# Kernel tuning notes

Measured on AMD Instinct MI355X. Metric: run time of the kernel, lower is better.

## Reference

```python
import jax, jax.numpy as jnp
import numpy as np

N_NODES = 50000
N_EDGES = 400000
N_GRAPHS = 128
D_IN = 768
D_HID = 256
D_OUT = 256
EPS_COS = 1e-8
EPS_BN = 1e-5
NEG_SLOPE = 0.2  # PyG GATConv default


def setup_inputs() -> dict:
    key = jax.random.key(0)
    ks = jax.random.split(key, 16)
    inp = {
        "claim_emb": jax.random.normal(ks[0], (N_GRAPHS, D_IN), dtype=jnp.float32),
        "x": jax.random.normal(ks[1], (N_NODES, D_IN), dtype=jnp.float32),
        "edge_index": jax.random.randint(ks[2], (2, N_EDGES), 0, N_NODES, dtype=jnp.int64 if jax.config.jax_enable_x64 else jnp.int32),
        "node_batch": jnp.sort(jax.random.randint(ks[3], (N_NODES,), 0, N_GRAPHS, dtype=jnp.int64 if jax.config.jax_enable_x64 else jnp.int32)),
        # GAT layer 1 (768 -> 256, single head)
        "W1": jax.random.normal(ks[4], (D_IN, D_HID), dtype=jnp.float32) * (1.0 / np.sqrt(D_IN)),
        "a_src1": jax.random.normal(ks[5], (D_HID,), dtype=jnp.float32) * 0.1,
        "a_dst1": jax.random.normal(ks[6], (D_HID,), dtype=jnp.float32) * 0.1,
        "b1": jnp.zeros((D_HID,), dtype=jnp.float32),
        # GAT layer 2 (256 -> 256)
        "W2": jax.random.normal(ks[7], (D_HID, D_OUT), dtype=jnp.float32) * (1.0 / np.sqrt(D_HID)),
        "a_src2": jax.random.normal(ks[8], (D_OUT,), dtype=jnp.float32) * 0.1,
        "a_dst2": jax.random.normal(ks[9], (D_OUT,), dtype=jnp.float32) * 0.1,
        "b2": jnp.zeros((D_OUT,), dtype=jnp.float32),
        # BatchNorm after layer 1
        "bn_gamma": jnp.ones((D_HID,), dtype=jnp.float32),
        "bn_beta": jnp.zeros((D_HID,), dtype=jnp.float32),
        # classifier: (gnn_out + claim_dim) -> 1
        "clf_W": jax.random.normal(ks[10], (D_OUT + D_IN, 1), dtype=jnp.float32) * (1.0 / np.sqrt(D_OUT + D_IN)),
        "clf_b": jnp.zeros((1,), dtype=jnp.float32),
    }
    return inp


def _gat_conv(x, src, dst, n_nodes, W, a_src, a_dst, b):
    """PyG GATConv, heads=1, concat=True, self-loops already appended to src/dst."""
    h = x @ W                                  # [N, H]
    alpha_s = h @ a_src                        # [N]
    alpha_d = h @ a_dst                        # [N]
    e = jax.nn.leaky_relu(alpha_s[src] + alpha_d[dst], NEG_SLOPE)  # [E]
    # segment softmax over edges grouped by destination node
    m = jax.ops.segment_max(e, dst, num_segments=n_nodes)          # [N]
    ex = jnp.exp(e - m[dst])
    denom = jax.ops.segment_sum(ex, dst, num_segments=n_nodes)     # [N]
    attn = ex / denom[dst]                                         # [E]
    out = jax.ops.segment_sum(h[src] * attn[:, None], dst, num_segments=n_nodes)
    return out + b


def reference(claim_emb, x, edge_index, node_batch,
              W1, a_src1, a_dst1, b1, W2, a_src2, a_dst2, b2,
              bn_gamma, bn_beta, clf_W, clf_b):
    n_nodes = x.shape[0]
    n_graphs = claim_emb.shape[0]

    # relevance weighting: cosine similarity between claim (per node's graph) and node feature
    ce = claim_emb[node_batch]                                      # [N, 768]
    dot = jnp.sum(ce * x, axis=-1)
    norm = jnp.linalg.norm(ce, axis=-1) * jnp.linalg.norm(x, axis=-1)
    rel = dot / jnp.maximum(norm, EPS_COS)                          # [N]
    h = x * rel[:, None]

    # add self loops (PyG GATConv default)
    loops = jnp.arange(n_nodes, dtype=edge_index.dtype)
    src = jnp.concatenate([edge_index[0], loops])
    dst = jnp.concatenate([edge_index[1], loops])

    # layer 1: GAT -> BatchNorm (training-mode batch stats) -> ReLU
    h = _gat_conv(h, src, dst, n_nodes, W1, a_src1, a_dst1, b1)
    mu = jnp.mean(h, axis=0)
    var = jnp.var(h, axis=0)
    h = (h - mu) / jnp.sqrt(var + EPS_BN) * bn_gamma + bn_beta
    h = jax.nn.relu(h)

    # layer 2: GAT -> ReLU
    h = _gat_conv(h, src, dst, n_nodes, W2, a_src2, a_dst2, b2)
    h = jax.nn.relu(h)

    # global mean pool per graph
    sums = jax.ops.segment_sum(h, node_batch, num_segments=n_graphs)            # [B, 256]
    counts = jax.ops.segment_sum(jnp.ones((n_nodes,), h.dtype), node_batch, num_segments=n_graphs)
    pooled = sums / jnp.maximum(counts, 1.0)[:, None]

    combined = jnp.concatenate([pooled, claim_emb], axis=1)                     # [B, 256+768]
    out = combined @ clf_W + clf_b                                              # [B, 1]
    return out[:, 0]
```

## Files before the change

### kernel.cpp

```cpp
#include <hip/hip_runtime.h>
#include <hip/hip_bf16.h>

#define N_NODES  50000
#define N_EDGES  400000
#define E_TOT    450000
#define N_GRAPHS 128
#define D_IN     768
#define D_HID    256

typedef __hip_bfloat16 bf16;
typedef __attribute__((ext_vector_type(8))) short short8;
typedef __attribute__((ext_vector_type(4))) short short4v;
typedef __attribute__((ext_vector_type(4))) float f32x4;

__device__ __forceinline__ float b2f(bf16 v) { return __bfloat162float(v); }
__device__ __forceinline__ float us2f(unsigned short u) { return __uint_as_float((unsigned)u << 16); }
__device__ __forceinline__ int clampN(int v) { return min(max(v, 0), N_NODES - 1); }
__device__ __forceinline__ short f2bs(float f) {
  unsigned u = __float_as_uint(f);
  return (short)((u + 0x7FFFu + ((u >> 16) & 1u)) >> 16);
}

__device__ __forceinline__ void gload_lds16(const void* g, void* l) {
  __builtin_amdgcn_global_load_lds(
      (const __attribute__((address_space(1))) void*)g,
      (__attribute__((address_space(3))) void*)l, 16, 0, 0);
}

__device__ __forceinline__ float waveReduceSum(float v) {
#pragma unroll
  for (int o = 32; o > 0; o >>= 1) v += __shfl_down(v, o);
  return v;
}

__device__ __forceinline__ float blockReduce256(float v, volatile float* buf4) {
  int lane = threadIdx.x & 63, wid = threadIdx.x >> 6;
  v = waveReduceSum(v);
  if (lane == 0) buf4[wid] = v;
  __syncthreads();
  float s = buf4[0] + buf4[1] + buf4[2] + buf4[3];
  __syncthreads();
  return s;
}

__global__ __launch_bounds__(256) void detect_idx_kernel(
    const int* __restrict__ edge32, int* __restrict__ flagNZ) {
  int t = threadIdx.x;
  int nz = 0;
#pragma unroll
  for (int i = 0; i < 4; ++i) {
    int idx = 2 * (t + i * 256) + 1;
    if (edge32[idx] != 0) nz = 1;
  }
  if (nz) atomicOr(flagNZ, 1);
}

__global__ __launch_bounds__(256) void normalize_idx_kernel(
    const void* __restrict__ edge, const void* __restrict__ nbin,
    const int* __restrict__ flagNZ,
    int* __restrict__ src32, int* __restrict__ dst32, int* __restrict__ nb32) {
  bool is64 = (*flagNZ == 0);
  long i = (long)blockIdx.x * 256 + threadIdx.x;
  const int*       e32 = (const int*)edge;
  const long long* e64 = (const long long*)edge;
  const int*       n32 = (const int*)nbin;
  const long long* n64 = (const long long*)nbin;
  if (i < N_EDGES) {
    src32[i] = clampN(is64 ? (int)e64[i] : e32[i]);
    dst32[i] = clampN(is64 ? (int)e64[N_EDGES + i] : e32[N_EDGES + i]);
  }
  long j = i - N_EDGES;
  if (j >= 0 && j < N_NODES)
    nb32[j] = min(max(is64 ? (int)n64[j] : n32[j], 0), N_GRAPHS - 1);
}

__global__ __launch_bounds__(256) void hist_kernel(
    const int* __restrict__ dst, int* __restrict__ deg) {
  int i = blockIdx.x * 256 + threadIdx.x;
  if (i >= E_TOT) return;
  int d = (i < N_EDGES) ? dst[i] : (i - N_EDGES);
  atomicAdd(&deg[d], 1);
}

#define SCAN_VPT 4
#define SCAN_BLK (256 * SCAN_VPT)
#define SCAN_NB  ((N_NODES + SCAN_BLK - 1) / SCAN_BLK)

__global__ __launch_bounds__(256) void scan_local_kernel(
    const int* __restrict__ deg, int* __restrict__ incl, int* __restrict__ blockSums) {
  __shared__ int wsum[4];
  int lane = threadIdx.x & 63, wid = threadIdx.x >> 6;
  int tbase = blockIdx.x * SCAN_BLK + threadIdx.x * SCAN_VPT;
  int v[SCAN_VPT];
  int s = 0;
#pragma unroll
  for (int j = 0; j < SCAN_VPT; ++j) {
    int i = tbase + j;
    v[j] = (i < N_NODES) ? deg[i] : 0;
    s += v[j];
  }
  int sc = s;
#pragma unroll
  for (int o = 1; o < 64; o <<= 1) {
    int t = __shfl_up(sc, o);
    if (lane >= o) sc += t;
  }
  if (lane == 63) wsum[wid] = sc;
  __syncthreads();
  int woff = 0;
  for (int w = 0; w < wid; ++w) woff += wsum[w];
  int run = woff + sc - s;
#pragma unroll
  for (int j = 0; j < SCAN_VPT; ++j) {
    run += v[j];
    int i = tbase + j;
    if (i < N_NODES) incl[i] = run;
  }
  if (threadIdx.x == 255)
    blockSums[blockIdx.x] = woff + sc;
}

__global__ __launch_bounds__(256) void scan_spine_kernel(int* __restrict__ bs) {
  __shared__ int wsum[4];
  int lane = threadIdx.x & 63, wid = threadIdx.x >> 6;
  int v = (threadIdx.x < SCAN_NB) ? bs[threadIdx.x] : 0;
  int sc = v;
#pragma unroll
  for (int o = 1; o < 64; o <<= 1) {
    int t = __shfl_up(sc, o);
    if (lane >= o) sc += t;
  }
  if (lane == 63) wsum[wid] = sc;
  __syncthreads();
  int woff = 0;
  for (int w = 0; w < wid; ++w) woff += wsum[w];
  if (threadIdx.x < SCAN_NB) bs[threadIdx.x] = woff + sc - v;
}

__global__ __launch_bounds__(256) void scan_add_kernel(
    const int* __restrict__ deg, const int* __restrict__ incl,
    const int* __restrict__ blockOffs,
    int* __restrict__ rowptr, int* __restrict__ pos) {
  int i = blockIdx.x * 256 + threadIdx.x;
  if (i >= N_NODES) return;
  int ic = incl[i] + blockOffs[i / SCAN_BLK];
  rowptr[i + 1] = ic;
  pos[i] = ic - deg[i];
  if (i == 0) rowptr[0] = 0;
}

__global__ __launch_bounds__(256) void scatter_kernel(
    const int* __restrict__ src, const int* __restrict__ dst,
    int* __restrict__ pos, int* __restrict__ srcS) {
  int i = blockIdx.x * 256 + threadIdx.x;
  if (i >= E_TOT) return;
  int s, d;
  if (i < N_EDGES) { s = src[i]; d = dst[i]; } else { s = d = i - N_EDGES; }
  int j = atomicAdd(&pos[d], 1);
  srcS[j] = s;
}

__global__ __launch_bounds__(256) void convert_wt_kernel(
    const float* __restrict__ W, short* __restrict__ WT, int K, int N) {
  int i = blockIdx.x * 256 + threadIdx.x;
  if (i >= K * N) return;
  int n = i / K, k = i - n * K;
  WT[i] = f2bs(W[(size_t)k * N + n]);
}

__global__ __launch_bounds__(256) void rel_conv_kernel(
    const float* __restrict__ x, const float* __restrict__ claim,
    const int* __restrict__ nb, short* __restrict__ Abf) {
  __shared__ float buf[4];
  int n = blockIdx.x;
  int g = nb[n];
  const float* xr = x + (size_t)n * D_IN;
  const float* cr = claim + (size_t)g * D_IN;
  float xv[3];
  float dot = 0.f, nx = 0.f, nc = 0.f;
#pragma unroll
  for (int i = 0; i < 3; ++i) {
    int d = threadIdx.x + i * 256;
    xv[i] = xr[d];
    float cv = cr[d];
    dot += xv[i] * cv; nx += xv[i] * xv[i]; nc += cv * cv;
  }
  dot = blockReduce256(dot, buf);
  nx  = blockReduce256(nx, buf);
  nc  = blockReduce256(nc, buf);
  float rel = dot / fmaxf(sqrtf(nx) * sqrtf(nc), 1e-8f);
#pragma unroll
  for (int i = 0; i < 3; ++i)
    Abf[(size_t)n * D_IN + threadIdx.x + i * 256] = f2bs(xv[i] * rel);
}

__global__ __launch_bounds__(256) void bn_conv_kernel(
    const float* __restrict__ agg, const float* __restrict__ scale,
    const float* __restrict__ shift, short* __restrict__ A2) {
  int i = blockIdx.x * 256 + threadIdx.x;
  f32x4 v = ((const f32x4*)agg)[i];
  int col = (i << 2) & (D_HID - 1);
  short4v o;
#pragma unroll
  for (int j = 0; j < 4; ++j) {
    float t = fmaxf(v[j] * scale[col + j] + shift[col + j], 0.f);
    o[j] = f2bs(t);
  }
  ((short4v*)A2)[i] = o;
}

#define GEMM_BK 32
__global__ __launch_bounds__(256) void mfma_gemm_bf16_kernel(
    const short* __restrict__ Abf, const short* __restrict__ BT,
    const float* __restrict__ aS, const float* __restrict__ aD,
    float* __restrict__ alphaS, float* __restrict__ alphaD,
    bf16* __restrict__ C, int M, int K) {
  __shared__ short As[4096];
  __shared__ short Bs[4096];
  int tid = threadIdx.x;
  int wave = tid >> 6, lane = tid & 63;
  int l16 = lane & 15, quadL = lane >> 4;
  int wr = wave >> 1, wc = wave & 1;
  int mBase = (blockIdx.x >> 1) * 128;
  int nBase = (blockIdx.x & 1) * 128;

  const short* gA[2];
  const short* gB[2];
  int ldsOff[2];
#pragma unroll
  for (int r = 0; r < 2; ++r) {
    int slot = r * 256 + tid;
    int mt = slot >> 6, m16 = (slot >> 2) & 15, quad = slot & 3;
    int rowA = min(mBase + mt * 16 + m16, M - 1);
    gA[r] = Abf + (size_t)rowA * K + quad * 8;
    gB[r] = BT + (size_t)(nBase + mt * 16 + m16) * K + quad * 8;
    ldsOff[r] = (r * 256 + wave * 64) * 8;
  }
  int aOff[4], bOff[4];
#pragma unroll
  for (int i = 0; i < 4; ++i) {
    aOff[i] = (wr * 4 + i) * 512 + l16 * 32 + quadL * 8;
    bOff[i] = (wc * 4 + i) * 512 + l16 * 32 + quadL * 8;
  }

  f32x4 acc[4][4] = {};

  for (int k0 = 0; k0 < K; k0 += GEMM_BK) {
#pragma unroll
    for (int r = 0; r < 2; ++r) {
      gload_lds16(gA[r] + k0, As + ldsOff[r]);
      gload_lds16(gB[r] + k0, Bs + ldsOff[r]);
    }
    __syncthreads();
    short8 af[4], bfv[4];
#pragma unroll
    for (int i = 0; i < 4; ++i) af[i] = *(const short8*)(As + aOff[i]);
#pragma unroll
    for (int j = 0; j < 4; ++j) bfv[j] = *(const short8*)(Bs + bOff[j]);
#pragma unroll
    for (int i = 0; i < 4; ++i)
#pragma unroll
      for (int j = 0; j < 4; ++j)
        acc[i][j] = __builtin_amdgcn_mfma_f32_16x16x32_bf16(af[i], bfv[j], acc[i][j], 0, 0, 0);
    __syncthreads();
  }

  float asv[4], adv[4];
#pragma unroll
  for (int j = 0; j < 4; ++j) {
    int col = nBase + (wc * 4 + j) * 16 + l16;
    asv[j] = aS[col]; adv[j] = aD[col];
  }
#pragma unroll
  for (int i = 0; i < 4; ++i) {
    int m0 = mBase + (wr * 4 + i) * 16 + quadL * 4;
#pragma unroll
    for (int r = 0; r < 4; ++r) {
      int m = m0 + r;
      float ss = acc[i][0][r] * asv[0] + acc[i][1][r] * asv[1] +
                 acc[i][2][r] * asv[2] + acc[i][3][r] * asv[3];
      float dd = acc[i][0][r] * adv[0] + acc[i][1][r] * adv[1] +
                 acc[i][2][r] * adv[2] + acc[i][3][r] * adv[3];
#pragma unroll
      for (int o = 1; o < 16; o <<= 1) {
        ss += __shfl_xor(ss, o);
        dd += __shfl_xor(dd, o);
      }
      if (m < M) {
        if (l16 == 0) { atomicAdd(&alphaS[m], ss); atomicAdd(&alphaD[m], dd); }
#pragma unroll
        for (int j = 0; j < 4; ++j)
          C[(size_t)m * D_HID + nBase + (wc * 4 + j) * 16 + l16] =
              __float2bfloat16(acc[i][j][r]);
      }
    }
  }
}

__global__ __launch_bounds__(256) void gat_agg_kernel(
    const int* __restrict__ rowptr, const int* __restrict__ srcS,
    const float* __restrict__ as_, const float* __restrict__ ad_,
    const bf16* __restrict__ h, float* __restrict__ agg) {
  int wid = threadIdx.x >> 6, lane = threadIdx.x & 63;
  int n = blockIdx.x * 4 + wid;
  if (n >= N_NODES) return;
  int start = rowptr[n], end = rowptr[n + 1];
  float adn = ad_[n];
  float m = -1e30f;
  for (int j0 = start; j0 < end; j0 += 64) {
    int j = j0 + lane;
    if (j < end) {
      float e = as_[srcS[j]] + adn;
      e = e > 0.f ? e : 0.2f * e;
      m = fmaxf(m, e);
    }
  }
#pragma unroll
  for (int o = 32; o > 0; o >>= 1) m = fmaxf(m, __shfl_xor(m, o));
  float ssum = 0.f;
  for (int j0 = start; j0 < end; j0 += 64) {
    int j = j0 + lane;
    if (j < end) {
      float e = as_[srcS[j]] + adn;
      e = e > 0.f ? e : 0.2f * e;
      ssum += __expf(e - m);
    }
  }
#pragma unroll
  for (int o = 32; o > 0; o >>= 1) ssum += __shfl_xor(ssum, o);
  float inv = 1.f / ssum;
  float a0 = 0.f, a1 = 0.f, a2 = 0.f, a3 = 0.f;
  const unsigned short* hp = (const unsigned short*)h;
  for (int j = start; j < end; ++j) {
    int s = srcS[j];
    float e = as_[s] + adn;
    e = e > 0.f ? e : 0.2f * e;
    float attn = __expf(e - m) * inv;
    const ushort4 hv = *(const ushort4*)(hp + (size_t)s * D_HID + lane * 4);
    a0 += us2f(hv.x) * attn;
    a1 += us2f(hv.y) * attn;
    a2 += us2f(hv.z) * attn;
    a3 += us2f(hv.w) * attn;
  }
  float4 o4 = {a0, a1, a2, a3};
  *(float4*)(agg + (size_t)n * D_HID + lane * 4) = o4;
}

__global__ __launch_bounds__(256) void bn_stats_kernel(
    const float* __restrict__ h, float* __restrict__ sums, float* __restrict__ sumsq) {
  int col = threadIdx.x;
  float s = 0.f, q = 0.f;
  for (int r = blockIdx.x; r < N_NODES; r += gridDim.x) {
    float v = h[(size_t)r * D_HID + col];
    s += v; q += v * v;
  }
  atomicAdd(&sums[col], s);
  atomicAdd(&sumsq[col], q);
}

__global__ __launch_bounds__(256) void bn_finalize_kernel(
    const float* __restrict__ sums, const float* __restrict__ sumsq,
    const float* __restrict__ gamma, const float* __restrict__ beta,
    float* __restrict__ scale, float* __restrict__ shift) {
  int c = threadIdx.x;
  float mu = sums[c] / N_NODES;
  float var = fmaxf(sumsq[c] / N_NODES - mu * mu, 0.f);
  float sc = gamma[c] * rsqrtf(var + 1e-5f);
  scale[c] = sc;
  shift[c] = beta[c] - mu * sc;
}

__global__ __launch_bounds__(256) void pool_kernel(
    const float* __restrict__ h, const float* __restrict__ bias2,
    const int* __restrict__ nb, float* __restrict__ pooled) {
  int col = threadIdx.x;
  float bias = bias2[col];
  int chunk = (N_NODES + gridDim.x - 1) / gridDim.x;
  int r0 = blockIdx.x * chunk;
  int r1 = min(N_NODES, r0 + chunk);
  float acc = 0.f; int cur = -1;
  for (int r = r0; r < r1; ++r) {
    int g = nb[r];
    if (g != cur) {
      if (cur >= 0) atomicAdd(&pooled[(size_t)cur * D_HID + col], acc);
      acc = 0.f; cur = g;
    }
    acc += fmaxf(h[(size_t)r * D_HID + col] + bias, 0.f);
  }
  if (cur >= 0) atomicAdd(&pooled[(size_t)cur * D_HID + col], acc);
}

__global__ __launch_bounds__(256) void count_kernel(
    const int* __restrict__ nb, float* __restrict__ counts) {
  __shared__ int cnt[N_GRAPHS];
  for (int i = threadIdx.x; i < N_GRAPHS; i += 256) cnt[i] = 0;
  __syncthreads();
  int n = blockIdx.x * 256 + threadIdx.x;
  if (n < N_NODES) atomicAdd(&cnt[nb[n]], 1);
  __syncthreads();
  for (int i = threadIdx.x; i < N_GRAPHS; i += 256)
    if (cnt[i]) atomicAdd(&counts[i], (float)cnt[i]);
}

__global__ __launch_bounds__(256) void clf_kernel(
    const float* __restrict__ pooled, const float* __restrict__ counts,
    const float* __restrict__ claim, const float* __restrict__ clfW,
    const float* __restrict__ clfb, float* __restrict__ out) {
  __shared__ float buf[4];
  int g = blockIdx.x;
  float inv = 1.f / fmaxf(counts[g], 1.f);
  float p = 0.f;
  for (int d = threadIdx.x; d < (D_HID + D_IN); d += 256) {
    float w = clfW[d];
    float v = (d < D_HID) ? pooled[(size_t)g * D_HID + d] * inv
                          : claim[(size_t)g * D_IN + (d - D_HID)];
    p += v * w;
  }
  p = blockReduce256(p, buf);
  if (threadIdx.x == 0) out[g] = p + clfb[0];
}

extern "C" void kernel_launch(void* const* d_in, const int* in_sizes, int n_in,
                              void* d_out, int out_size, void* d_ws, size_t ws_size,
                              hipStream_t stream) {
  const float* claim = (const float*)d_in[0];
  const float* x     = (const float*)d_in[1];
  const void*  edge  = d_in[2];
  const void*  nbin  = d_in[3];
  const float* W1    = (const float*)d_in[4];
  const float* as1   = (const float*)d_in[5];
  const float* ad1   = (const float*)d_in[6];
  const float* W2    = (const float*)d_in[8];
  const float* as2   = (const float*)d_in[9];
  const float* ad2   = (const float*)d_in[10];
  const float* b2v   = (const float*)d_in[11];
  const float* gamma = (const float*)d_in[12];
  const float* beta  = (const float*)d_in[13];
  const float* clfW  = (const float*)d_in[14];
  const float* clfb  = (const float*)d_in[15];
  float* out = (float*)d_out;

  char* wsb = (char*)d_ws;
  size_t off = 0;
  auto alloc = [&](size_t bytes) -> char* {
    char* p = wsb + off;
    off = (off + bytes + 255) & ~(size_t)255;
    return p;
  };
  int*   flagNZ = (int*)alloc(sizeof(int));
  int*   src32  = (int*)alloc((size_t)N_EDGES * sizeof(int));
  int*   dst32  = (int*)alloc((size_t)N_EDGES * sizeof(int));
  int*   nb32   = (int*)alloc((size_t)N_NODES * sizeof(int));
  int*   deg    = (int*)alloc((size_t)N_NODES * sizeof(int));
  int*   rowptr = (int*)alloc((size_t)(N_NODES + 1) * sizeof(int));
  int*   pos    = (int*)alloc((size_t)N_NODES * sizeof(int));
  int*   incl   = (int*)alloc((size_t)N_NODES * sizeof(int));
  int*   bsums  = (int*)alloc((size_t)SCAN_NB * sizeof(int));
  int*   srcS   = (int*)alloc((size_t)E_TOT * sizeof(int));
  short* W1T    = (short*)alloc((size_t)D_IN * D_HID * sizeof(short));
  short* W2T    = (short*)alloc((size_t)D_HID * D_HID * sizeof(short));
  float* alphas = (float*)alloc((size_t)N_NODES * sizeof(float));
  float* alphad = (float*)alloc((size_t)N_NODES * sizeof(float));
  float* bnsums = (float*)alloc(D_HID * sizeof(float));
  float* bnsq   = (float*)alloc(D_HID * sizeof(float));
  float* bnscale= (float*)alloc(D_HID * sizeof(float));
  float* bnshift= (float*)alloc(D_HID * sizeof(float));
  float* pooled = (float*)alloc((size_t)N_GRAPHS * D_HID * sizeof(float));
  float* counts = (float*)alloc((size_t)N_GRAPHS * sizeof(float));
  float* agg    = (float*)alloc((size_t)N_NODES * D_HID * sizeof(float));
  bf16*  h      = (bf16*) alloc((size_t)N_NODES * D_HID * sizeof(bf16));
  short* Abf    = (short*)alloc((size_t)N_NODES * D_IN * sizeof(short));
  short* A2     = Abf;

  hipMemsetAsync(flagNZ, 0, sizeof(int), stream);
  detect_idx_kernel<<<1, 256, 0, stream>>>((const int*)edge, flagNZ);
  normalize_idx_kernel<<<(N_EDGES + N_NODES + 255) / 256, 256, 0, stream>>>(
      edge, nbin, flagNZ, src32, dst32, nb32);
  hipMemsetAsync(deg, 0, (size_t)N_NODES * sizeof(int), stream);
  int egrid = (E_TOT + 255) / 256;
  hist_kernel<<<egrid, 256, 0, stream>>>(dst32, deg);
  scan_local_kernel<<<SCAN_NB, 256, 0, stream>>>(deg, incl, bsums);
  scan_spine_kernel<<<1, 256, 0, stream>>>(bsums);
  scan_add_kernel<<<(N_NODES + 255) / 256, 256, 0, stream>>>(deg, incl, bsums, rowptr, pos);
  scatter_kernel<<<egrid, 256, 0, stream>>>(src32, dst32, pos, srcS);

  convert_wt_kernel<<<(D_IN * D_HID + 255) / 256, 256, 0, stream>>>(W1, W1T, D_IN, D_HID);
  convert_wt_kernel<<<(D_HID * D_HID + 255) / 256, 256, 0, stream>>>(W2, W2T, D_HID, D_HID);

  hipMemsetAsync(bnsums, 0, D_HID * 4, stream);
  hipMemsetAsync(bnsq, 0, D_HID * 4, stream);
  hipMemsetAsync(pooled, 0, (size_t)N_GRAPHS * D_HID * 4, stream);
  hipMemsetAsync(counts, 0, (size_t)N_GRAPHS * 4, stream);

  int gemmGrid = ((N_NODES + 127) / 128) * 2;

  rel_conv_kernel<<<N_NODES, 256, 0, stream>>>(x, claim, nb32, Abf);
  hipMemsetAsync(alphas, 0, (size_t)N_NODES * 4, stream);
  hipMemsetAsync(alphad, 0, (size_t)N_NODES * 4, stream);
  mfma_gemm_bf16_kernel<<<gemmGrid, 256, 0, stream>>>(
      Abf, W1T, as1, ad1, alphas, alphad, h, N_NODES, D_IN);
  gat_agg_kernel<<<N_NODES / 4, 256, 0, stream>>>(rowptr, srcS, alphas, alphad, h, agg);

  bn_stats_kernel<<<256, 256, 0, stream>>>(agg, bnsums, bnsq);
  bn_finalize_kernel<<<1, 256, 0, stream>>>(bnsums, bnsq, gamma, beta, bnscale, bnshift);

  bn_conv_kernel<<<(N_NODES * D_HID / 4 + 255) / 256, 256, 0, stream>>>(
      agg, bnscale, bnshift, A2);
  hipMemsetAsync(alphas, 0, (size_t)N_NODES * 4, stream);
  hipMemsetAsync(alphad, 0, (size_t)N_NODES * 4, stream);
  mfma_gemm_bf16_kernel<<<gemmGrid, 256, 0, stream>>>(
      A2, W2T, as2, ad2, alphas, alphad, h, N_NODES, D_HID);
  gat_agg_kernel<<<N_NODES / 4, 256, 0, stream>>>(rowptr, srcS, alphas, alphad, h, agg);

  pool_kernel<<<256, 256, 0, stream>>>(agg, b2v, nb32, pooled);
  count_kernel<<<(N_NODES + 255) / 256, 256, 0, stream>>>(nb32, counts);
  clf_kernel<<<N_GRAPHS, 256, 0, stream>>>(pooled, counts, claim, clfW, clfb, out);
}
```

Measured before the change: 690.5 us.

## Fold memsets and tiny kernels into neighbors; cache first-chunk edge scores in GAT aggregation

Removes all hipMemsetAsync calls and several tiny kernels (scan spine, BN finalize, count, second weight convert) by folding their zeroing and compute into adjacent kernels. The scan spine becomes a per-block reduction in scan_add, BN scale/shift is recomputed inline in bn_conv, and per-graph counts come from a binary search over the sorted batch vector. In gat_agg the first 64 edges' source indices and scores are kept in registers and broadcast via shuffles, avoiding repeat srcS/alpha loads for most nodes. Normalization is deferred to the end. The cost is redundant per-element BN math and reliance on node_batch being sorted.

```diff
diff --git a/kernel.cpp b/kernel.cpp
--- a/kernel.cpp
+++ b/kernel.cpp
@@ -45,6 +45,8 @@
 
 __global__ __launch_bounds__(256) void detect_idx_kernel(
     const int* __restrict__ edge32, int* __restrict__ flagNZ) {
+  if (threadIdx.x == 0) *flagNZ = 0;
+  __syncthreads();
   int t = threadIdx.x;
   int nz = 0;
 #pragma unroll
@@ -58,13 +60,15 @@
 __global__ __launch_bounds__(256) void normalize_idx_kernel(
     const void* __restrict__ edge, const void* __restrict__ nbin,
     const int* __restrict__ flagNZ,
-    int* __restrict__ src32, int* __restrict__ dst32, int* __restrict__ nb32) {
+    int* __restrict__ src32, int* __restrict__ dst32, int* __restrict__ nb32,
+    int* __restrict__ deg) {
   bool is64 = (*flagNZ == 0);
   long i = (long)blockIdx.x * 256 + threadIdx.x;
   const int*       e32 = (const int*)edge;
   const long long* e64 = (const long long*)edge;
   const int*       n32 = (const int*)nbin;
   const long long* n64 = (const long long*)nbin;
+  if (i < N_NODES) deg[i] = 0;
   if (i < N_EDGES) {
     src32[i] = clampN(is64 ? (int)e64[i] : e32[i]);
     dst32[i] = clampN(is64 ? (int)e64[N_EDGES + i] : e32[N_EDGES + i]);
@@ -120,30 +124,22 @@
     blockSums[blockIdx.x] = woff + sc;
 }
 
-__global__ __launch_bounds__(256) void scan_spine_kernel(int* __restrict__ bs) {
-  __shared__ int wsum[4];
-  int lane = threadIdx.x & 63, wid = threadIdx.x >> 6;
-  int v = (threadIdx.x < SCAN_NB) ? bs[threadIdx.x] : 0;
-  int sc = v;
-#pragma unroll
-  for (int o = 1; o < 64; o <<= 1) {
-    int t = __shfl_up(sc, o);
-    if (lane >= o) sc += t;
-  }
-  if (lane == 63) wsum[wid] = sc;
-  __syncthreads();
-  int woff = 0;
-  for (int w = 0; w < wid; ++w) woff += wsum[w];
-  if (threadIdx.x < SCAN_NB) bs[threadIdx.x] = woff + sc - v;
-}
-
 __global__ __launch_bounds__(256) void scan_add_kernel(
     const int* __restrict__ deg, const int* __restrict__ incl,
-    const int* __restrict__ blockOffs,
+    const int* __restrict__ bsums,
     int* __restrict__ rowptr, int* __restrict__ pos) {
+  __shared__ int offSh;
+  int sb = blockIdx.x >> 2;
+  if (threadIdx.x < 64) {
+    int v = (threadIdx.x < sb) ? bsums[threadIdx.x] : 0;
+#pragma unroll
+    for (int o = 32; o > 0; o >>= 1) v += __shfl_down(v, o);
+    if (threadIdx.x == 0) offSh = v;
+  }
+  __syncthreads();
   int i = blockIdx.x * 256 + threadIdx.x;
   if (i >= N_NODES) return;
-  int ic = incl[i] + blockOffs[i / SCAN_BLK];
+  int ic = incl[i] + offSh;
   rowptr[i + 1] = ic;
   pos[i] = ic - deg[i];
   if (i == 0) rowptr[0] = 0;
@@ -161,18 +157,29 @@
 }
 
 __global__ __launch_bounds__(256) void convert_wt_kernel(
-    const float* __restrict__ W, short* __restrict__ WT, int K, int N) {
+    const float* __restrict__ W1, const float* __restrict__ W2,
+    short* __restrict__ W1T, short* __restrict__ W2T) {
   int i = blockIdx.x * 256 + threadIdx.x;
-  if (i >= K * N) return;
-  int n = i / K, k = i - n * K;
-  WT[i] = f2bs(W[(size_t)k * N + n]);
+  if (i < D_IN * D_HID) {
+    int n = i / D_IN, k = i - n * D_IN;
+    W1T[i] = f2bs(W1[(size_t)k * D_HID + n]);
+  }
+  int j = i - D_IN * D_HID;
+  if (j >= 0 && j < D_HID * D_HID) {
+    int n = j / D_HID, k = j - n * D_HID;
+    W2T[j] = f2bs(W2[(size_t)k * D_HID + n]);
+  }
 }
 
 __global__ __launch_bounds__(256) void rel_conv_kernel(
     const float* __restrict__ x, const float* __restrict__ claim,
-    const int* __restrict__ nb, short* __restrict__ Abf) {
+    const int* __restrict__ nb, short* __restrict__ Abf,
+    float* __restrict__ alphas, float* __restrict__ alphad,
+    float* __restrict__ bnsums, float* __restrict__ bnsq) {
   __shared__ float buf[4];
   int n = blockIdx.x;
+  if (threadIdx.x == 0) { alphas[n] = 0.f; alphad[n] = 0.f; }
+  if (n == 0) { bnsums[threadIdx.x] = 0.f; bnsq[threadIdx.x] = 0.f; }
   int g = nb[n];
   const float* xr = x + (size_t)n * D_IN;
   const float* cr = claim + (size_t)g * D_IN;
@@ -195,15 +202,24 @@
 }
 
 __global__ __launch_bounds__(256) void bn_conv_kernel(
-    const float* __restrict__ agg, const float* __restrict__ scale,
-    const float* __restrict__ shift, short* __restrict__ A2) {
+    const float* __restrict__ agg, const float* __restrict__ sums,
+    const float* __restrict__ sumsq, const float* __restrict__ gamma,
+    const float* __restrict__ beta, short* __restrict__ A2,
+    float* __restrict__ alphas, float* __restrict__ alphad,
+    float* __restrict__ pooled) {
   int i = blockIdx.x * 256 + threadIdx.x;
+  if ((i & 63) == 0) { int n = i >> 6; alphas[n] = 0.f; alphad[n] = 0.f; }
+  if (i < N_GRAPHS * D_HID) pooled[i] = 0.f;
   f32x4 v = ((const f32x4*)agg)[i];
   int col = (i << 2) & (D_HID - 1);
   short4v o;
 #pragma unroll
   for (int j = 0; j < 4; ++j) {
-    float t = fmaxf(v[j] * scale[col + j] + shift[col + j], 0.f);
+    float mu  = sums[col + j] * (1.f / N_NODES);
+    float var = fmaxf(sumsq[col + j] * (1.f / N_NODES) - mu * mu, 0.f);
+    float sc  = gamma[col + j] * rsqrtf(var + 1e-5f);
+    float sh  = beta[col + j] - mu * sc;
+    float t = fmaxf(v[j] * sc + sh, 0.f);
     o[j] = f2bs(t);
   }
   ((short4v*)A2)[i] = o;
@@ -305,9 +321,17 @@
   int n = blockIdx.x * 4 + wid;
   if (n >= N_NODES) return;
   int start = rowptr[n], end = rowptr[n + 1];
+  int deg = end - start;
   float adn = ad_[n];
-  float m = -1e30f;
-  for (int j0 = start; j0 < end; j0 += 64) {
+  int sidx = 0;
+  float e0 = -1e30f;
+  if (lane < deg) {
+    sidx = srcS[start + lane];
+    float e = as_[sidx] + adn;
+    e0 = e > 0.f ? e : 0.2f * e;
+  }
+  float m = e0;
+  for (int j0 = start + 64; j0 < end; j0 += 64) {
     int j = j0 + lane;
     if (j < end) {
       float e = as_[srcS[j]] + adn;
@@ -317,8 +341,8 @@
   }
 #pragma unroll
   for (int o = 32; o > 0; o >>= 1) m = fmaxf(m, __shfl_xor(m, o));
-  float ssum = 0.f;
-  for (int j0 = start; j0 < end; j0 += 64) {
+  float ssum = (lane < deg) ? __expf(e0 - m) : 0.f;
+  for (int j0 = start + 64; j0 < end; j0 += 64) {
     int j = j0 + lane;
     if (j < end) {
       float e = as_[srcS[j]] + adn;
@@ -328,21 +352,32 @@
   }
 #pragma unroll
   for (int o = 32; o > 0; o >>= 1) ssum += __shfl_xor(ssum, o);
-  float inv = 1.f / ssum;
   float a0 = 0.f, a1 = 0.f, a2 = 0.f, a3 = 0.f;
   const unsigned short* hp = (const unsigned short*)h;
-  for (int j = start; j < end; ++j) {
+  int c0 = min(deg, 64);
+  for (int t = 0; t < c0; ++t) {
+    int s = __shfl(sidx, t);
+    float ev = __shfl(e0, t);
+    float w = __expf(ev - m);
+    const ushort4 hv = *(const ushort4*)(hp + (size_t)s * D_HID + lane * 4);
+    a0 += us2f(hv.x) * w;
+    a1 += us2f(hv.y) * w;
+    a2 += us2f(hv.z) * w;
+    a3 += us2f(hv.w) * w;
+  }
+  for (int j = start + 64; j < end; ++j) {
     int s = srcS[j];
     float e = as_[s] + adn;
     e = e > 0.f ? e : 0.2f * e;
-    float attn = __expf(e - m) * inv;
+    float w = __expf(e - m);
     const ushort4 hv = *(const ushort4*)(hp + (size_t)s * D_HID + lane * 4);
-    a0 += us2f(hv.x) * attn;
-    a1 += us2f(hv.y) * attn;
-    a2 += us2f(hv.z) * attn;
-    a3 += us2f(hv.w) * attn;
-  }
-  float4 o4 = {a0, a1, a2, a3};
+    a0 += us2f(hv.x) * w;
+    a1 += us2f(hv.y) * w;
+    a2 += us2f(hv.z) * w;
+    a3 += us2f(hv.w) * w;
+  }
+  float inv = 1.f / ssum;
+  float4 o4 = {a0 * inv, a1 * inv, a2 * inv, a3 * inv};
   *(float4*)(agg + (size_t)n * D_HID + lane * 4) = o4;
 }
 
@@ -356,18 +391,6 @@
   }
   atomicAdd(&sums[col], s);
   atomicAdd(&sumsq[col], q);
-}
-
-__global__ __launch_bounds__(256) void bn_finalize_kernel(
-    const float* __restrict__ sums, const float* __restrict__ sumsq,
-    const float* __restrict__ gamma, const float* __restrict__ beta,
-    float* __restrict__ scale, float* __restrict__ shift) {
-  int c = threadIdx.x;
-  float mu = sums[c] / N_NODES;
-  float var = fmaxf(sumsq[c] / N_NODES - mu * mu, 0.f);
-  float sc = gamma[c] * rsqrtf(var + 1e-5f);
-  scale[c] = sc;
-  shift[c] = beta[c] - mu * sc;
 }
 
 __global__ __launch_bounds__(256) void pool_kernel(
@@ -390,25 +413,22 @@
   if (cur >= 0) atomicAdd(&pooled[(size_t)cur * D_HID + col], acc);
 }
 
-__global__ __launch_bounds__(256) void count_kernel(
-    const int* __restrict__ nb, float* __restrict__ counts) {
-  __shared__ int cnt[N_GRAPHS];
-  for (int i = threadIdx.x; i < N_GRAPHS; i += 256) cnt[i] = 0;
-  __syncthreads();
-  int n = blockIdx.x * 256 + threadIdx.x;
-  if (n < N_NODES) atomicAdd(&cnt[nb[n]], 1);
-  __syncthreads();
-  for (int i = threadIdx.x; i < N_GRAPHS; i += 256)
-    if (cnt[i]) atomicAdd(&counts[i], (float)cnt[i]);
-}
-
 __global__ __launch_bounds__(256) void clf_kernel(
-    const float* __restrict__ pooled, const float* __restrict__ counts,
+    const float* __restrict__ pooled, const int* __restrict__ nb,
     const float* __restrict__ claim, const float* __restrict__ clfW,
     const float* __restrict__ clfb, float* __restrict__ out) {
   __shared__ float buf[4];
+  __shared__ int cntSh;
   int g = blockIdx.x;
-  float inv = 1.f / fmaxf(counts[g], 1.f);
+  if (threadIdx.x == 0) {
+    int lo = 0, hi = N_NODES;
+    while (lo < hi) { int mid = (lo + hi) >> 1; if (nb[mid] < g) lo = mid + 1; else hi = mid; }
+    int lb = lo; hi = N_NODES;
+    while (lo < hi) { int mid = (lo + hi) >> 1; if (nb[mid] <= g) lo = mid + 1; else hi = mid; }
+    cntSh = lo - lb;
+  }
+  __syncthreads();
+  float inv = 1.f / fmaxf((float)cntSh, 1.f);
   float p = 0.f;
   for (int d = threadIdx.x; d < (D_HID + D_IN); d += 256) {
     float w = clfW[d];
@@ -463,56 +483,40 @@
   float* alphad = (float*)alloc((size_t)N_NODES * sizeof(float));
   float* bnsums = (float*)alloc(D_HID * sizeof(float));
   float* bnsq   = (float*)alloc(D_HID * sizeof(float));
-  float* bnscale= (float*)alloc(D_HID * sizeof(float));
-  float* bnshift= (float*)alloc(D_HID * sizeof(float));
   float* pooled = (float*)alloc((size_t)N_GRAPHS * D_HID * sizeof(float));
-  float* counts = (float*)alloc((size_t)N_GRAPHS * sizeof(float));
   float* agg    = (float*)alloc((size_t)N_NODES * D_HID * sizeof(float));
   bf16*  h      = (bf16*) alloc((size_t)N_NODES * D_HID * sizeof(bf16));
   short* Abf    = (short*)alloc((size_t)N_NODES * D_IN * sizeof(short));
   short* A2     = Abf;
 
-  hipMemsetAsync(flagNZ, 0, sizeof(int), stream);
   detect_idx_kernel<<<1, 256, 0, stream>>>((const int*)edge, flagNZ);
   normalize_idx_kernel<<<(N_EDGES + N_NODES + 255) / 256, 256, 0, stream>>>(
-      edge, nbin, flagNZ, src32, dst32, nb32);
-  hipMemsetAsync(deg, 0, (size_t)N_NODES * sizeof(int), stream);
+      edge, nbin, flagNZ, src32, dst32, nb32, deg);
   int egrid = (E_TOT + 255) / 256;
   hist_kernel<<<egrid, 256, 0, stream>>>(dst32, deg);
   scan_local_kernel<<<SCAN_NB, 256, 0, stream>>>(deg, incl, bsums);
-  scan_spine_kernel<<<1, 256, 0, stream>>>(bsums);
   scan_add_kernel<<<(N_NODES + 255) / 256, 256, 0, stream>>>(deg, incl, bsums, rowptr, pos);
   scatter_kernel<<<egrid, 256, 0, stream>>>(src32, dst32, pos, srcS);
 
-  convert_wt_kernel<<<(D_IN * D_HID + 255) / 256, 256, 0, stream>>>(W1, W1T, D_IN, D_HID);
-  convert_wt_kernel<<<(D_HID * D_HID + 255) / 256, 256, 0, stream>>>(W2, W2T, D_HID, D_HID);
-
-  hipMemsetAsync(bnsums, 0, D_HID * 4, stream);
-  hipMemsetAsync(bnsq, 0, D_HID * 4, stream);
-  hipMemsetAsync(pooled, 0, (size_t)N_GRAPHS * D_HID * 4, stream);
-  hipMemsetAsync(counts, 0, (size_t)N_GRAPHS * 4, stream);
+  convert_wt_kernel<<<(D_IN * D_HID + D_HID * D_HID + 255) / 256, 256, 0, stream>>>(
+      W1, W2, W1T, W2T);
 
   int gemmGrid = ((N_NODES + 127) / 128) * 2;
 
-  rel_conv_kernel<<<N_NODES, 256, 0, stream>>>(x, claim, nb32, Abf);
-  hipMemsetAsync(alphas, 0, (size_t)N_NODES * 4, stream);
-  hipMemsetAsync(alphad, 0, (size_t)N_NODES * 4, stream);
+  rel_conv_kernel<<<N_NODES, 256, 0, stream>>>(
+      x, claim, nb32, Abf, alphas, alphad, bnsums, bnsq);
   mfma_gemm_bf16_kernel<<<gemmGrid, 256, 0, stream>>>(
       Abf, W1T, as1, ad1, alphas, alphad, h, N_NODES, D_IN);
   gat_agg_kernel<<<N_NODES / 4, 256, 0, stream>>>(rowptr, srcS, alphas, alphad, h, agg);
 
   bn_stats_kernel<<<256, 256, 0, stream>>>(agg, bnsums, bnsq);
-  bn_finalize_kernel<<<1, 256, 0, stream>>>(bnsums, bnsq, gamma, beta, bnscale, bnshift);
 
   bn_conv_kernel<<<(N_NODES * D_HID / 4 + 255) / 256, 256, 0, stream>>>(
-      agg, bnscale, bnshift, A2);
-  hipMemsetAsync(alphas, 0, (size_t)N_NODES * 4, stream);
-  hipMemsetAsync(alphad, 0, (size_t)N_NODES * 4, stream);
+      agg, bnsums, bnsq, gamma, beta, A2, alphas, alphad, pooled);
   mfma_gemm_bf16_kernel<<<gemmGrid, 256, 0, stream>>>(
       A2, W2T, as2, ad2, alphas, alphad, h, N_NODES, D_HID);
   gat_agg_kernel<<<N_NODES / 4, 256, 0, stream>>>(rowptr, srcS, alphas, alphad, h, agg);
 
   pool_kernel<<<256, 256, 0, stream>>>(agg, b2v, nb32, pooled);
-  count_kernel<<<(N_NODES + 255) / 256, 256, 0, stream>>>(nb32, counts);
-  clf_kernel<<<N_GRAPHS, 256, 0, stream>>>(pooled, counts, claim, clfW, clfb, out);
-}
+  clf_kernel<<<N_GRAPHS, 256, 0, stream>>>(pooled, nb32, claim, clfW, clfb, out);
+}
```

Result: faster. 627.0 us (-9.2%).
